# Kernel optimization log

Measured on AMD Instinct MI355X. Metric: run time of the kernel, lower is better.

The kernel has to match this reference:

```python
import jax, jax.numpy as jnp
import numpy as np

EMBD_DIM = 512
HIDDEN_DIM = 512
TARGET_DIM = 128
BATCH = 64
MAX_SET = 2048


def setup_inputs() -> dict:
    key = jax.random.key(0)
    ks = jax.random.split(key, 10)
    E, H, T = EMBD_DIM, HIDDEN_DIM, TARGET_DIM
    s = lambda fan_in: 1.0 / np.sqrt(fan_in)
    return {
        "words": jax.random.normal(ks[0], (BATCH, MAX_SET, E), dtype=jnp.float32),
        # attention_layer: Linear(2E -> H) followed by tanh; v: (H, 1)
        "W_att": jax.random.uniform(ks[1], (2 * E, H), jnp.float32, -s(2 * E), s(2 * E)),
        "b_att": jax.random.uniform(ks[2], (H,), jnp.float32, -s(2 * E), s(2 * E)),
        "v": jax.random.normal(ks[3], (H, 1), dtype=jnp.float32),
        # pred_net: Linear(E,H) -> ReLU -> Linear(H,H) -> ReLU -> Linear(H,T)
        "W1": jax.random.uniform(ks[4], (E, H), jnp.float32, -s(E), s(E)),
        "b1": jax.random.uniform(ks[5], (H,), jnp.float32, -s(E), s(E)),
        "W2": jax.random.uniform(ks[6], (H, H), jnp.float32, -s(H), s(H)),
        "b2": jax.random.uniform(ks[7], (H,), jnp.float32, -s(H), s(H)),
        "W3": jax.random.uniform(ks[8], (H, T), jnp.float32, -s(H), s(H)),
        "b3": jax.random.uniform(ks[9], (T,), jnp.float32, -s(H), s(H)),
    }


def reference(words, W_att, b_att, v, W1, b1, W2, b2, W3, b3):
    # words: [B, S, E]. A row is "valid" iff its feature-sum is nonzero
    # (matches words.sum(2).abs().sign() in the torch code).
    mask = jnp.sign(jnp.abs(words.sum(-1)))           # [B, S], 0/1 float
    lengths = mask.sum(axis=1, keepdims=True)          # [B, 1]
    # context = mean over valid rows (padded rows are exactly zero)
    context = words.sum(axis=1, keepdims=True) / lengths[..., None]  # [B, 1, E]
    context = jnp.broadcast_to(context, words.shape)   # [B, S, E]

    x = jnp.concatenate([words, context], axis=-1)     # [B, S, 2E]
    h = jnp.tanh(x @ W_att + b_att)                    # [B, S, H]
    scores = (h @ v)[..., 0]                           # [B, S]

    # per-segment softmax over valid rows only (masked_select + per-batch
    # Softmax in the original == masked softmax here)
    scores = jnp.where(mask > 0, scores, jnp.full_like(scores, -1e30))
    attn = jax.nn.softmax(scores, axis=1)              # [B, S]

    rep = jnp.einsum("bs,bse->be", attn, words)        # [B, E]

    pred = jax.nn.relu(rep @ W1 + b1)
    pred = jax.nn.relu(pred @ W2 + b2)
    pred = pred @ W3 + b3                              # [B, T]
    return pred
```

## Files before the change

### kernel.cpp

```cpp
#include <hip/hip_runtime.h>
#include <hip/hip_bf16.h>
#include <hip/hip_fp16.h>
#include <math.h>

#define B 64
#define S 2048
#define E 512
#define HD 512
#define TD 128
#define M_TOT (B*S)
#define NCHUNK (M_TOT/128)

#define OFF_MASK   0
#define OFF_CTXP   (OFF_MASK + B*S)
#define OFF_LENP   (OFF_CTXP + 8*B*E)
#define OFF_CB     (OFF_LENP + 8*B)
#define OFF_PP     (OFF_CB + B*HD)
#define OFF_ML     (OFF_PP + NCHUNK*E)
#define OFF_LL     (OFF_ML + NCHUNK)
#define OFF_WPK    (OFF_LL + NCHUNK)

typedef __attribute__((ext_vector_type(8))) short short8;
typedef __attribute__((ext_vector_type(4))) float f32x4;

__device__ inline unsigned int f2hu(float x) {
    __half h = __float2half(x);
    unsigned short u; __builtin_memcpy(&u, &h, 2); return (unsigned int)u;
}

__device__ inline float fast_tanh(float x) {
    float a = fabsf(x);
    float e = __expf(-2.0f * a);
    float r = (1.0f - e) / (1.0f + e);
    return copysignf(r, x);
}

__global__ __launch_bounds__(256)
void k0_pack(const float* __restrict__ W_att, unsigned short* __restrict__ Wpk)
{
    int tid = blockIdx.x*256 + threadIdx.x;
    int e = tid >> 9, h = tid & 511;
    float w = W_att[(size_t)e*HD + h];
    int kstep = e >> 5, kb = (e >> 3) & 3, j = e & 7, f = h >> 4, l15 = h & 15;
    size_t dst = ((((size_t)kstep*32 + f)*64) + kb*16 + l15)*8 + j;
    Wpk[dst] = (unsigned short)f2hu(w);
}

__global__ __launch_bounds__(256)
void k1_maskcol(const float* __restrict__ words, float* __restrict__ mask,
                float* __restrict__ ctxp, float* __restrict__ lenp)
{
    int bid = blockIdx.x;
    int b = bid >> 3, ch = bid & 7;
    int t = threadIdx.x;
    int w = t >> 6, l = t & 63;
    __shared__ __align__(16) float colred[4][E];
    __shared__ float lenred[4];
    const float* base = words + (size_t)(b * S + ch * 256) * E;
    float4 c0 = make_float4(0.f,0.f,0.f,0.f), c1 = make_float4(0.f,0.f,0.f,0.f);
    float wlen = 0.0f;
    for (int r = w; r < 256; r += 4) {
        const float* row = base + (size_t)r * E;
        float4 a  = *(const float4*)(row + 4*l);
        float4 bb = *(const float4*)(row + 256 + 4*l);
        float rs = a.x+a.y+a.z+a.w + bb.x+bb.y+bb.z+bb.w;
        #pragma unroll
        for (int m = 1; m < 64; m <<= 1) rs += __shfl_xor(rs, m);
        c0.x += a.x;  c0.y += a.y;  c0.z += a.z;  c0.w += a.w;
        c1.x += bb.x; c1.y += bb.y; c1.z += bb.z; c1.w += bb.w;
        if (l == 0) {
            float mv = (rs != 0.0f) ? 1.0f : 0.0f;
            mask[(size_t)b*S + ch*256 + r] = mv;
            wlen += mv;
        }
    }
    *(float4*)&colred[w][4*l]       = c0;
    *(float4*)&colred[w][256 + 4*l] = c1;
    if (l == 0) lenred[w] = wlen;
    __syncthreads();
    float s1 = colred[0][t]+colred[1][t]+colred[2][t]+colred[3][t];
    float s2 = colred[0][t+256]+colred[1][t+256]+colred[2][t+256]+colred[3][t+256];
    size_t o = ((size_t)ch * B + b) * E;
    ctxp[o + t]       = s1;
    ctxp[o + t + 256] = s2;
    if (t == 0) lenp[ch*B + b] = lenred[0]+lenred[1]+lenred[2]+lenred[3];
}

__global__ __launch_bounds__(256)
void k2_cb(const float* __restrict__ W_att, const float* __restrict__ b_att,
           const float* __restrict__ ctxp, const float* __restrict__ lenp,
           float* __restrict__ cb)
{
    int bid = blockIdx.x;
    int b = bid >> 1, hc = bid & 1;
    int t = threadIdx.x;
    __shared__ float ctxL[E];
    float len = 0.f;
    #pragma unroll
    for (int k = 0; k < 8; ++k) len += lenp[k*B + b];
    float inv = 1.0f / len;
    for (int c = t; c < E; c += 256) {
        float sv = 0.f;
        #pragma unroll
        for (int k = 0; k < 8; ++k) sv += ctxp[((size_t)k*B + b)*E + c];
        ctxL[c] = sv * inv;
    }
    __syncthreads();
    int h = hc*256 + t;
    const float* Wb = W_att + (size_t)E * HD;
    float a0 = b_att[h], a1 = 0.f, a2 = 0.f, a3 = 0.f;
    #pragma unroll 4
    for (int e = 0; e < E; e += 4) {
        a0 += ctxL[e]   * Wb[(size_t)e*HD + h];
        a1 += ctxL[e+1] * Wb[(size_t)(e+1)*HD + h];
        a2 += ctxL[e+2] * Wb[(size_t)(e+2)*HD + h];
        a3 += ctxL[e+3] * Wb[(size_t)(e+3)*HD + h];
    }
    cb[(size_t)b*HD + h] = (a0 + a1) + (a2 + a3);
}

__global__ __launch_bounds__(512, 2)
void k3_scores(const float* __restrict__ words,
               const unsigned short* __restrict__ Wpk,
               const float* __restrict__ cb, const float* __restrict__ v,
               const float* __restrict__ mask,
               float* __restrict__ Pp, float* __restrict__ Ml, float* __restrict__ Ll)
{
    __shared__ __align__(16) unsigned char smem[16384];
    int mt = blockIdx.x;
    int m0 = mt * 128;
    int b  = m0 >> 11;
    int t = threadIdx.x;
    int lane = t & 63, wid = t >> 6;
    int wr = wid >> 2, wc = wid & 3;

    f32x4 acc[4][8];
    #pragma unroll
    for (int i = 0; i < 4; ++i)
        #pragma unroll
        for (int j = 0; j < 8; ++j) acc[i][j] = (f32x4)0.0f;

    int sF = (t >> 6) & 7, skb = (t >> 4) & 3, sl15 = t & 15;
    int srow = sF*16 + sl15;
    const float* aSrc = words + (size_t)(m0 + srow)*E + skb*8;

    const unsigned short* bBase = Wpk + (((size_t)(wc*8))*64 + lane)*8;
#define LDB(kst,cf) (*(const short8*)(bBase + ((size_t)(kst)*32 + (cf))*512))

    float4 pa0, pa1, qa0, qa1;
#define LOADA(P0, P1, s) do { const float* _s = aSrc + (s)*32; \
        P0 = *(const float4*)(_s); P1 = *(const float4*)(_s + 4); } while(0)
#define STAGEA(buf, P0, P1) do { \
        unsigned int u0 = f2hu(P0.x) | (f2hu(P0.y) << 16); \
        unsigned int u1 = f2hu(P0.z) | (f2hu(P0.w) << 16); \
        unsigned int u2 = f2hu(P1.x) | (f2hu(P1.y) << 16); \
        unsigned int u3 = f2hu(P1.z) | (f2hu(P1.w) << 16); \
        *(uint4*)&(buf)[t*16] = make_uint4(u0, u1, u2, u3); } while(0)

    unsigned char* sm0 = smem;
    unsigned char* sm1 = smem + 8192;

    short8 bA[8], bB[8];

    LOADA(pa0, pa1, 0);
    STAGEA(sm0, pa0, pa1);
    LOADA(pa0, pa1, 1);
    LOADA(qa0, qa1, 2);
    #pragma unroll
    for (int cf = 0; cf < 8; ++cf) bA[cf] = LDB(0, cf);
    __syncthreads();

#define KBODY(k, BUFC, BUFN, P0, P1, BCUR, BNEXT) do { \
        short8 ah[4]; \
        _Pragma("unroll") \
        for (int rf = 0; rf < 4; ++rf) \
            ah[rf] = *(const short8*)&(BUFC)[(wr*4 + rf)*1024 + lane*16]; \
        if ((k) < 15) { \
            _Pragma("unroll") \
            for (int cf = 0; cf < 8; ++cf) BNEXT[cf] = LDB((k)+1, cf); \
            STAGEA(BUFN, P0, P1); \
        } \
        if ((k) < 13) LOADA(P0, P1, (k) + 3); \
        _Pragma("unroll") \
        for (int cf = 0; cf < 8; ++cf) { \
            _Pragma("unroll") \
            for (int rf = 0; rf < 4; ++rf) \
                acc[rf][cf] = __builtin_amdgcn_mfma_f32_16x16x32_f16(ah[rf], BCUR[cf], acc[rf][cf], 0, 0, 0); \
        } \
        __syncthreads(); } while(0)

    KBODY( 0, sm0, sm1, pa0, pa1, bA, bB);
    KBODY( 1, sm1, sm0, qa0, qa1, bB, bA);
    KBODY( 2, sm0, sm1, pa0, pa1, bA, bB);
    KBODY( 3, sm1, sm0, qa0, qa1, bB, bA);
    KBODY( 4, sm0, sm1, pa0, pa1, bA, bB);
    KBODY( 5, sm1, sm0, qa0, qa1, bB, bA);
    KBODY( 6, sm0, sm1, pa0, pa1, bA, bB);
    KBODY( 7, sm1, sm0, qa0, qa1, bB, bA);
    KBODY( 8, sm0, sm1, pa0, pa1, bA, bB);
    KBODY( 9, sm1, sm0, qa0, qa1, bB, bA);
    KBODY(10, sm0, sm1, pa0, pa1, bA, bB);
    KBODY(11, sm1, sm0, qa0, qa1, bB, bA);
    KBODY(12, sm0, sm1, pa0, pa1, bA, bB);
    KBODY(13, sm1, sm0, qa0, qa1, bB, bA);
    KBODY(14, sm0, sm1, pa0, pa1, bA, bB);
    KBODY(15, sm1, sm0, qa0, qa1, bB, bA);
#undef KBODY
#undef LOADA
#undef STAGEA
#undef LDB

    float ssum[4][4];
    #pragma unroll
    for (int i = 0; i < 4; ++i)
        #pragma unroll
        for (int rr = 0; rr < 4; ++rr) ssum[i][rr] = 0.f;

    #pragma unroll
    for (int cf = 0; cf < 8; ++cf) {
        int col = wc*128 + cf*16 + (lane & 15);
        float cbv = cb[(size_t)b*HD + col];
        float vv  = v[col];
        #pragma unroll
        for (int rf = 0; rf < 4; ++rf)
            #pragma unroll
            for (int rr = 0; rr < 4; ++rr)
                ssum[rf][rr] += fast_tanh(acc[rf][cf][rr] + cbv) * vv;
    }
    #pragma unroll
    for (int m = 1; m < 16; m <<= 1)
        #pragma unroll
        for (int rf = 0; rf < 4; ++rf)
            #pragma unroll
            for (int rr = 0; rr < 4; ++rr)
                ssum[rf][rr] += __shfl_xor(ssum[rf][rr], m);

    float* fsm = (float*)smem;
    float* scr   = fsm;
    float* scm   = fsm + 512;
    float* wrow  = fsm + 640;
    float* redv  = fsm + 768;

    if ((lane & 15) == 0) {
        #pragma unroll
        for (int rf = 0; rf < 4; ++rf)
            #pragma unroll
            for (int rr = 0; rr < 4; ++rr)
                scr[wc*128 + wr*64 + rf*16 + (lane >> 4)*4 + rr] = ssum[rf][rr];
    }
    __syncthreads();

    if (t < 128) {
        float val = (scr[t] + scr[128 + t]) + (scr[256 + t] + scr[384 + t]);
        float mk = mask[(size_t)m0 + t];
        scm[t] = (mk > 0.0f) ? val : -1e30f;
    }
    __syncthreads();
    if (t < 64) {
        float m1 = fmaxf(scm[t], scm[t + 64]);
        #pragma unroll
        for (int mm = 1; mm < 64; mm <<= 1) m1 = fmaxf(m1, __shfl_xor(m1, mm));
        if (t == 0) redv[0] = m1;
    }
    __syncthreads();
    float m_c = redv[0];
    if (t < 128) wrow[t] = __expf(scm[t] - m_c);
    __syncthreads();
    if (t < 64) {
        float s1 = wrow[t] + wrow[t + 64];
        #pragma unroll
        for (int mm = 1; mm < 64; mm <<= 1) s1 += __shfl_xor(s1, mm);
        if (t == 0) redv[1] = s1;
    }

    float P = 0.f;
    const float* wbase = words + (size_t)m0*E + t;
    #pragma unroll 8
    for (int r2 = 0; r2 < 128; ++r2)
        P = fmaf(wrow[r2], wbase[(size_t)r2*E], P);
    __syncthreads();
    Pp[(size_t)mt*E + t] = P;
    if (t == 0) { Ml[mt] = m_c; Ll[mt] = redv[1]; }
}

__global__ __launch_bounds__(256)
void k5_mlp(const float* __restrict__ Pp, const float* __restrict__ Ml,
            const float* __restrict__ Ll,
            const float* __restrict__ W1, const float* __restrict__ b1,
            const float* __restrict__ W2, const float* __restrict__ b2,
            const float* __restrict__ W3, const float* __restrict__ b3,
            float* __restrict__ out)
{
    int b = blockIdx.x;
    int t = threadIdx.x;
    __shared__ float xL[HD];
    __shared__ float yL[HD];
    __shared__ float wf[16];

    if (t == 0) {
        float M = -3e38f;
        #pragma unroll
        for (int c = 0; c < 16; ++c) M = fmaxf(M, Ml[b*16 + c]);
        float den = 0.f;
        #pragma unroll
        for (int c = 0; c < 16; ++c) den += __expf(Ml[b*16 + c] - M) * Ll[b*16 + c];
        float inv = 1.0f / den;
        #pragma unroll
        for (int c = 0; c < 16; ++c) wf[c] = __expf(Ml[b*16 + c] - M) * inv;
    }
    __syncthreads();

    #pragma unroll
    for (int oo = 0; oo < 2; ++oo) {
        int e = oo*256 + t;
        float sv = 0.f;
        #pragma unroll
        for (int c = 0; c < 16; ++c)
            sv += wf[c] * Pp[(size_t)(b*16 + c)*E + e];
        xL[e] = sv;
    }
    __syncthreads();
    #pragma unroll
    for (int oo = 0; oo < 2; ++oo) {
        int h = oo*256 + t;
        float a0 = b1[h], a1 = 0.f, a2 = 0.f, a3 = 0.f;
        #pragma unroll 4
        for (int e = 0; e < E; e += 4) {
            a0 += xL[e]   * W1[(size_t)e*HD + h];
            a1 += xL[e+1] * W1[(size_t)(e+1)*HD + h];
            a2 += xL[e+2] * W1[(size_t)(e+2)*HD + h];
            a3 += xL[e+3] * W1[(size_t)(e+3)*HD + h];
        }
        yL[h] = fmaxf((a0 + a1) + (a2 + a3), 0.f);
    }
    __syncthreads();
    float l2v[2];
    #pragma unroll
    for (int oo = 0; oo < 2; ++oo) {
        int h = oo*256 + t;
        float a0 = b2[h], a1 = 0.f, a2 = 0.f, a3 = 0.f;
        #pragma unroll 4
        for (int e = 0; e < HD; e += 4) {
            a0 += yL[e]   * W2[(size_t)e*HD + h];
            a1 += yL[e+1] * W2[(size_t)(e+1)*HD + h];
            a2 += yL[e+2] * W2[(size_t)(e+2)*HD + h];
            a3 += yL[e+3] * W2[(size_t)(e+3)*HD + h];
        }
        l2v[oo] = fmaxf((a0 + a1) + (a2 + a3), 0.f);
    }
    __syncthreads();
    xL[t] = l2v[0]; xL[256 + t] = l2v[1];
    __syncthreads();
    if (t < TD) {
        float a0 = b3[t], a1 = 0.f, a2 = 0.f, a3 = 0.f;
        #pragma unroll 4
        for (int e = 0; e < HD; e += 4) {
            a0 += xL[e]   * W3[(size_t)e*TD + t];
            a1 += xL[e+1] * W3[(size_t)(e+1)*TD + t];
            a2 += xL[e+2] * W3[(size_t)(e+2)*TD + t];
            a3 += xL[e+3] * W3[(size_t)(e+3)*TD + t];
        }
        out[(size_t)b*TD + t] = (a0 + a1) + (a2 + a3);
    }
}

extern "C" void kernel_launch(void* const* d_in, const int* in_sizes, int n_in,
                              void* d_out, int out_size, void* d_ws, size_t ws_size,
                              hipStream_t stream)
{
    const float* words = (const float*)d_in[0];
    const float* W_att = (const float*)d_in[1];
    const float* b_att = (const float*)d_in[2];
    const float* v     = (const float*)d_in[3];
    const float* W1    = (const float*)d_in[4];
    const float* b1    = (const float*)d_in[5];
    const float* W2    = (const float*)d_in[6];
    const float* b2    = (const float*)d_in[7];
    const float* W3    = (const float*)d_in[8];
    const float* b3    = (const float*)d_in[9];
    (void)in_sizes; (void)n_in; (void)out_size; (void)ws_size;

    float* ws   = (float*)d_ws;
    float* mask = ws + OFF_MASK;
    float* ctxp = ws + OFF_CTXP;
    float* lenp = ws + OFF_LENP;
    float* cb   = ws + OFF_CB;
    float* Pp   = ws + OFF_PP;
    float* Ml   = ws + OFF_ML;
    float* Ll   = ws + OFF_LL;
    unsigned short* Wpk = (unsigned short*)(ws + OFF_WPK);
    float* out  = (float*)d_out;

    hipLaunchKernelGGL(k0_pack,    dim3(1024), dim3(256), 0, stream, W_att, Wpk);
    hipLaunchKernelGGL(k1_maskcol, dim3(B*8),  dim3(256), 0, stream, words, mask, ctxp, lenp);
    hipLaunchKernelGGL(k2_cb,      dim3(B*2),  dim3(256), 0, stream, W_att, b_att, ctxp, lenp, cb);
    hipLaunchKernelGGL(k3_scores,  dim3(1024), dim3(512), 0, stream, words, Wpk, cb, v, mask, Pp, Ml, Ll);
    hipLaunchKernelGGL(k5_mlp,     dim3(B),    dim3(256), 0, stream, Pp, Ml, Ll, W1, b1, W2, b2, W3, b3, out);
}
```

Measured before the change: 308.5 us.

## Stage whole fp32 words tile in LDS via direct global-to-LDS loads

The scores kernel now uses 64-row tiles and loads the full 64x512 fp32 words tile into a swizzled 128KB LDS buffer with global_load_lds. It converts to fp16 at fragment-read time instead of double-buffering fp16 k-slices through registers. The tile held in LDS is reused for the attention-weighted sum, so words is no longer re-read from global memory, and the per-iteration barriers go away. The cost is very large LDS use, which allows only one block per CU, half the MFMA work per B-fragment load, twice as many chunks to merge in the MLP kernel, and no overlap between the load phase and compute.

```diff
diff --git a/kernel.cpp b/kernel.cpp
--- a/kernel.cpp
+++ b/kernel.cpp
@@ -9,7 +9,8 @@
 #define HD 512
 #define TD 128
 #define M_TOT (B*S)
-#define NCHUNK (M_TOT/128)
+#define MTILE 64
+#define NCHUNK (M_TOT/MTILE)
 
 #define OFF_MASK   0
 #define OFF_CTXP   (OFF_MASK + B*S)
@@ -33,6 +34,19 @@
     float e = __expf(-2.0f * a);
     float r = (1.0f - e) / (1.0f + e);
     return copysignf(r, x);
+}
+
+#define GLOAD_LDS16(gpu, lds) \
+    __builtin_amdgcn_global_load_lds((__attribute__((address_space(1))) const void*)(gpu), \
+                                     (__attribute__((address_space(3))) void*)(lds), 16, 0, 0)
+
+__device__ inline short8 pack8h(const f32x4 lo, const f32x4 hi) {
+    union { short8 s; __half2 h[4]; } u;
+    u.h[0] = __float22half2_rn(make_float2(lo[0], lo[1]));
+    u.h[1] = __float22half2_rn(make_float2(lo[2], lo[3]));
+    u.h[2] = __float22half2_rn(make_float2(hi[0], hi[1]));
+    u.h[3] = __float22half2_rn(make_float2(hi[2], hi[3]));
+    return u.s;
 }
 
 __global__ __launch_bounds__(256)
@@ -126,93 +140,77 @@
                const float* __restrict__ mask,
                float* __restrict__ Pp, float* __restrict__ Ml, float* __restrict__ Ll)
 {
-    __shared__ __align__(16) unsigned char smem[16384];
+    __shared__ __align__(16) unsigned char smem[131072 + 2608];
     int mt = blockIdx.x;
-    int m0 = mt * 128;
+    int m0 = mt * MTILE;
     int b  = m0 >> 11;
     int t = threadIdx.x;
     int lane = t & 63, wid = t >> 6;
     int wr = wid >> 2, wc = wid & 3;
 
-    f32x4 acc[4][8];
-    #pragma unroll
-    for (int i = 0; i < 4; ++i)
+    f32x4 acc[2][8];
+    #pragma unroll
+    for (int i = 0; i < 2; ++i)
         #pragma unroll
         for (int j = 0; j < 8; ++j) acc[i][j] = (f32x4)0.0f;
 
-    int sF = (t >> 6) & 7, skb = (t >> 4) & 3, sl15 = t & 15;
-    int srow = sF*16 + sl15;
-    const float* aSrc = words + (size_t)(m0 + srow)*E + skb*8;
+    {
+        #pragma unroll
+        for (int ii = 0; ii < 16; ++ii) {
+            int i = wid*16 + ii;
+            int row = i >> 1;
+            int g = (((i & 1) << 6) | lane) ^ (row & 7);
+            const float* src = words + (size_t)(m0 + row)*E + g*4;
+            GLOAD_LDS16(src, &smem[i*1024]);
+        }
+    }
 
     const unsigned short* bBase = Wpk + (((size_t)(wc*8))*64 + lane)*8;
 #define LDB(kst,cf) (*(const short8*)(bBase + ((size_t)(kst)*32 + (cf))*512))
 
-    float4 pa0, pa1, qa0, qa1;
-#define LOADA(P0, P1, s) do { const float* _s = aSrc + (s)*32; \
-        P0 = *(const float4*)(_s); P1 = *(const float4*)(_s + 4); } while(0)
-#define STAGEA(buf, P0, P1) do { \
-        unsigned int u0 = f2hu(P0.x) | (f2hu(P0.y) << 16); \
-        unsigned int u1 = f2hu(P0.z) | (f2hu(P0.w) << 16); \
-        unsigned int u2 = f2hu(P1.x) | (f2hu(P1.y) << 16); \
-        unsigned int u3 = f2hu(P1.z) | (f2hu(P1.w) << 16); \
-        *(uint4*)&(buf)[t*16] = make_uint4(u0, u1, u2, u3); } while(0)
-
-    unsigned char* sm0 = smem;
-    unsigned char* sm1 = smem + 8192;
-
     short8 bA[8], bB[8];
-
-    LOADA(pa0, pa1, 0);
-    STAGEA(sm0, pa0, pa1);
-    LOADA(pa0, pa1, 1);
-    LOADA(qa0, qa1, 2);
     #pragma unroll
     for (int cf = 0; cf < 8; ++cf) bA[cf] = LDB(0, cf);
     __syncthreads();
 
-#define KBODY(k, BUFC, BUFN, P0, P1, BCUR, BNEXT) do { \
-        short8 ah[4]; \
+    int arow0 = wr*32 + (lane & 15);
+    int klane = ((lane >> 4) & 3) * 2;
+#define KBODY(k, BCUR, BNEXT) do { \
+        short8 ah[2]; \
         _Pragma("unroll") \
-        for (int rf = 0; rf < 4; ++rf) \
-            ah[rf] = *(const short8*)&(BUFC)[(wr*4 + rf)*1024 + lane*16]; \
+        for (int rf = 0; rf < 2; ++rf) { \
+            int row = arow0 + rf*16; \
+            int g0 = (k)*8 + klane; \
+            int swz = row & 7; \
+            f32x4 lo = *(const f32x4*)&smem[row*2048 + ((g0    ) ^ swz)*16]; \
+            f32x4 hi = *(const f32x4*)&smem[row*2048 + ((g0 + 1) ^ swz)*16]; \
+            ah[rf] = pack8h(lo, hi); \
+        } \
         if ((k) < 15) { \
             _Pragma("unroll") \
             for (int cf = 0; cf < 8; ++cf) BNEXT[cf] = LDB((k)+1, cf); \
-            STAGEA(BUFN, P0, P1); \
         } \
-        if ((k) < 13) LOADA(P0, P1, (k) + 3); \
         _Pragma("unroll") \
         for (int cf = 0; cf < 8; ++cf) { \
             _Pragma("unroll") \
-            for (int rf = 0; rf < 4; ++rf) \
+            for (int rf = 0; rf < 2; ++rf) \
                 acc[rf][cf] = __builtin_amdgcn_mfma_f32_16x16x32_f16(ah[rf], BCUR[cf], acc[rf][cf], 0, 0, 0); \
-        } \
-        __syncthreads(); } while(0)
-
-    KBODY( 0, sm0, sm1, pa0, pa1, bA, bB);
-    KBODY( 1, sm1, sm0, qa0, qa1, bB, bA);
-    KBODY( 2, sm0, sm1, pa0, pa1, bA, bB);
-    KBODY( 3, sm1, sm0, qa0, qa1, bB, bA);
-    KBODY( 4, sm0, sm1, pa0, pa1, bA, bB);
-    KBODY( 5, sm1, sm0, qa0, qa1, bB, bA);
-    KBODY( 6, sm0, sm1, pa0, pa1, bA, bB);
-    KBODY( 7, sm1, sm0, qa0, qa1, bB, bA);
-    KBODY( 8, sm0, sm1, pa0, pa1, bA, bB);
-    KBODY( 9, sm1, sm0, qa0, qa1, bB, bA);
-    KBODY(10, sm0, sm1, pa0, pa1, bA, bB);
-    KBODY(11, sm1, sm0, qa0, qa1, bB, bA);
-    KBODY(12, sm0, sm1, pa0, pa1, bA, bB);
-    KBODY(13, sm1, sm0, qa0, qa1, bB, bA);
-    KBODY(14, sm0, sm1, pa0, pa1, bA, bB);
-    KBODY(15, sm1, sm0, qa0, qa1, bB, bA);
+        } } while(0)
+
+    KBODY( 0, bA, bB);  KBODY( 1, bB, bA);
+    KBODY( 2, bA, bB);  KBODY( 3, bB, bA);
+    KBODY( 4, bA, bB);  KBODY( 5, bB, bA);
+    KBODY( 6, bA, bB);  KBODY( 7, bB, bA);
+    KBODY( 8, bA, bB);  KBODY( 9, bB, bA);
+    KBODY(10, bA, bB);  KBODY(11, bB, bA);
+    KBODY(12, bA, bB);  KBODY(13, bB, bA);
+    KBODY(14, bA, bB);  KBODY(15, bB, bA);
 #undef KBODY
-#undef LOADA
-#undef STAGEA
 #undef LDB
 
-    float ssum[4][4];
-    #pragma unroll
-    for (int i = 0; i < 4; ++i)
+    float ssum[2][4];
+    #pragma unroll
+    for (int i = 0; i < 2; ++i)
         #pragma unroll
         for (int rr = 0; rr < 4; ++rr) ssum[i][rr] = 0.f;
 
@@ -222,7 +220,7 @@
         float cbv = cb[(size_t)b*HD + col];
         float vv  = v[col];
         #pragma unroll
-        for (int rf = 0; rf < 4; ++rf)
+        for (int rf = 0; rf < 2; ++rf)
             #pragma unroll
             for (int rr = 0; rr < 4; ++rr)
                 ssum[rf][rr] += fast_tanh(acc[rf][cf][rr] + cbv) * vv;
@@ -230,57 +228,54 @@
     #pragma unroll
     for (int m = 1; m < 16; m <<= 1)
         #pragma unroll
-        for (int rf = 0; rf < 4; ++rf)
+        for (int rf = 0; rf < 2; ++rf)
             #pragma unroll
             for (int rr = 0; rr < 4; ++rr)
                 ssum[rf][rr] += __shfl_xor(ssum[rf][rr], m);
 
-    float* fsm = (float*)smem;
-    float* scr   = fsm;
-    float* scm   = fsm + 512;
-    float* wrow  = fsm + 640;
-    float* redv  = fsm + 768;
+    float* fsm  = (float*)(smem + 131072);
+    float* scr  = fsm;
+    float* scm  = fsm + 256;
+    float* wrow = fsm + 320;
+    float* redv = fsm + 384;
 
     if ((lane & 15) == 0) {
         #pragma unroll
-        for (int rf = 0; rf < 4; ++rf)
+        for (int rf = 0; rf < 2; ++rf)
             #pragma unroll
             for (int rr = 0; rr < 4; ++rr)
-                scr[wc*128 + wr*64 + rf*16 + (lane >> 4)*4 + rr] = ssum[rf][rr];
-    }
-    __syncthreads();
-
-    if (t < 128) {
-        float val = (scr[t] + scr[128 + t]) + (scr[256 + t] + scr[384 + t]);
+                scr[wc*64 + wr*32 + rf*16 + (lane >> 4)*4 + rr] = ssum[rf][rr];
+    }
+    __syncthreads();
+
+    if (t < 64) {
+        float val = (scr[t] + scr[64 + t]) + (scr[128 + t] + scr[192 + t]);
         float mk = mask[(size_t)m0 + t];
-        scm[t] = (mk > 0.0f) ? val : -1e30f;
-    }
-    __syncthreads();
-    if (t < 64) {
-        float m1 = fmaxf(scm[t], scm[t + 64]);
+        float x = (mk > 0.0f) ? val : -1e30f;
+        scm[t] = x;
+        float m1 = x;
         #pragma unroll
         for (int mm = 1; mm < 64; mm <<= 1) m1 = fmaxf(m1, __shfl_xor(m1, mm));
-        if (t == 0) redv[0] = m1;
-    }
-    __syncthreads();
-    float m_c = redv[0];
-    if (t < 128) wrow[t] = __expf(scm[t] - m_c);
-    __syncthreads();
-    if (t < 64) {
-        float s1 = wrow[t] + wrow[t + 64];
+        float wv = __expf(x - m1);
+        wrow[t] = wv;
+        float s1 = wv;
         #pragma unroll
         for (int mm = 1; mm < 64; mm <<= 1) s1 += __shfl_xor(s1, mm);
-        if (t == 0) redv[1] = s1;
-    }
-
-    float P = 0.f;
-    const float* wbase = words + (size_t)m0*E + t;
-    #pragma unroll 8
-    for (int r2 = 0; r2 < 128; ++r2)
-        P = fmaf(wrow[r2], wbase[(size_t)r2*E], P);
-    __syncthreads();
-    Pp[(size_t)mt*E + t] = P;
-    if (t == 0) { Ml[mt] = m_c; Ll[mt] = redv[1]; }
+        if (t == 0) { redv[0] = m1; redv[1] = s1; }
+    }
+    __syncthreads();
+
+    {
+        int g = t >> 2, w4 = (t & 3);
+        float P = 0.f;
+        #pragma unroll 8
+        for (int r2 = 0; r2 < 64; ++r2) {
+            const float* gp = (const float*)&smem[r2*2048 + ((g ^ (r2 & 7)) << 4)];
+            P = fmaf(wrow[r2], gp[w4], P);
+        }
+        Pp[(size_t)mt*E + t] = P;
+    }
+    if (t == 0) { Ml[mt] = redv[0]; Ll[mt] = redv[1]; }
 }
 
 __global__ __launch_bounds__(256)
@@ -295,18 +290,18 @@
     int t = threadIdx.x;
     __shared__ float xL[HD];
     __shared__ float yL[HD];
-    __shared__ float wf[16];
+    __shared__ float wf[32];
 
     if (t == 0) {
         float M = -3e38f;
         #pragma unroll
-        for (int c = 0; c < 16; ++c) M = fmaxf(M, Ml[b*16 + c]);
+        for (int c = 0; c < 32; ++c) M = fmaxf(M, Ml[b*32 + c]);
         float den = 0.f;
         #pragma unroll
-        for (int c = 0; c < 16; ++c) den += __expf(Ml[b*16 + c] - M) * Ll[b*16 + c];
+        for (int c = 0; c < 32; ++c) den += __expf(Ml[b*32 + c] - M) * Ll[b*32 + c];
         float inv = 1.0f / den;
         #pragma unroll
-        for (int c = 0; c < 16; ++c) wf[c] = __expf(Ml[b*16 + c] - M) * inv;
+        for (int c = 0; c < 32; ++c) wf[c] = __expf(Ml[b*32 + c] - M) * inv;
     }
     __syncthreads();
 
@@ -314,9 +309,9 @@
     for (int oo = 0; oo < 2; ++oo) {
         int e = oo*256 + t;
         float sv = 0.f;
-        #pragma unroll
-        for (int c = 0; c < 16; ++c)
-            sv += wf[c] * Pp[(size_t)(b*16 + c)*E + e];
+        #pragma unroll 8
+        for (int c = 0; c < 32; ++c)
+            sv += wf[c] * Pp[(size_t)(b*32 + c)*E + e];
         xL[e] = sv;
     }
     __syncthreads();
@@ -391,9 +386,9 @@
     unsigned short* Wpk = (unsigned short*)(ws + OFF_WPK);
     float* out  = (float*)d_out;
 
-    hipLaunchKernelGGL(k0_pack,    dim3(1024), dim3(256), 0, stream, W_att, Wpk);
-    hipLaunchKernelGGL(k1_maskcol, dim3(B*8),  dim3(256), 0, stream, words, mask, ctxp, lenp);
-    hipLaunchKernelGGL(k2_cb,      dim3(B*2),  dim3(256), 0, stream, W_att, b_att, ctxp, lenp, cb);
-    hipLaunchKernelGGL(k3_scores,  dim3(1024), dim3(512), 0, stream, words, Wpk, cb, v, mask, Pp, Ml, Ll);
-    hipLaunchKernelGGL(k5_mlp,     dim3(B),    dim3(256), 0, stream, Pp, Ml, Ll, W1, b1, W2, b2, W3, b3, out);
-}
+    hipLaunchKernelGGL(k0_pack,    dim3(1024),   dim3(256), 0, stream, W_att, Wpk);
+    hipLaunchKernelGGL(k1_maskcol, dim3(B*8),    dim3(256), 0, stream, words, mask, ctxp, lenp);
+    hipLaunchKernelGGL(k2_cb,      dim3(B*2),    dim3(256), 0, stream, W_att, b_att, ctxp, lenp, cb);
+    hipLaunchKernelGGL(k3_scores,  dim3(NCHUNK), dim3(512), 0, stream, words, Wpk, cb, v, mask, Pp, Ml, Ll);
+    hipLaunchKernelGGL(k5_mlp,     dim3(B),      dim3(256), 0, stream, Pp, Ml, Ll, W1, b1, W2, b2, W3, b3, out);
+}
```

After: 392.1 us. 1.27x slower.
